# Kernel tuning notes

Measured on AMD Instinct MI355X. Metric: run time of the kernel, lower is better.

## Reference

```python
import jax, jax.numpy as jnp
import numpy as np

N_HEADS = 8
EPS = 1e-5

def _mha(q_in, kv_in, wq, bq, wk, bk, wv, bv, wo, bo, causal):
    B, N, D = q_in.shape
    Dh = D // N_HEADS
    # projections (weights stored [in, out])
    Q = (q_in @ wq + bq).reshape(B, N, N_HEADS, Dh).swapaxes(1, 2)  # [B,H,N,Dh]
    K = (kv_in @ wk + bk).reshape(B, N, N_HEADS, Dh).swapaxes(1, 2)
    V = (kv_in @ wv + bv).reshape(B, N, N_HEADS, Dh).swapaxes(1, 2)
    scores = jnp.einsum('bhqd,bhkd->bhqk', Q, K) / jnp.sqrt(jnp.asarray(Dh, q_in.dtype))
    if causal:
        m = jnp.triu(jnp.ones((N, N), dtype=bool), k=1)
        scores = jnp.where(m, jnp.asarray(-jnp.inf, scores.dtype), scores)
    w = jax.nn.softmax(scores, axis=-1)
    attn = jnp.einsum('bhqk,bhkd->bhqd', w, V).swapaxes(1, 2).reshape(B, N, D)
    return attn @ wo + bo

def _ln(x, g, b):
    mu = jnp.mean(x, axis=-1, keepdims=True)
    var = jnp.var(x, axis=-1, keepdims=True)
    return (x - mu) / jnp.sqrt(var + EPS) * g + b

def setup_inputs() -> dict:
    key = jax.random.key(0)
    D, H, S = 512, 8, 4
    ks = jax.random.split(key, 32)
    def w(k, shape):
        return jax.random.normal(k, shape, dtype=jnp.float32) * 0.02
    inp = {
        'x': jax.random.normal(ks[0], (2, 2048, D), dtype=jnp.float32),
        'encoder_output': jax.random.normal(ks[1], (2, 2048, D), dtype=jnp.float32),
        # masked self-attention params
        'm_wq': w(ks[2], (D, D)), 'm_bq': jnp.zeros((D,), jnp.float32),
        'm_wk': w(ks[3], (D, D)), 'm_bk': jnp.zeros((D,), jnp.float32),
        'm_wv': w(ks[4], (D, D)), 'm_bv': jnp.zeros((D,), jnp.float32),
        'm_wo': w(ks[5], (D, D)), 'm_bo': jnp.zeros((D,), jnp.float32),
        # cross-attention params
        'c_wq': w(ks[6], (D, D)), 'c_bq': jnp.zeros((D,), jnp.float32),
        'c_wk': w(ks[7], (D, D)), 'c_bk': jnp.zeros((D,), jnp.float32),
        'c_wv': w(ks[8], (D, D)), 'c_bv': jnp.zeros((D,), jnp.float32),
        'c_wo': w(ks[9], (D, D)), 'c_bo': jnp.zeros((D,), jnp.float32),
        # layer norms
        'ln1_g': jnp.ones((D,), jnp.float32), 'ln1_b': jnp.zeros((D,), jnp.float32),
        'ln2_g': jnp.ones((D,), jnp.float32), 'ln2_b': jnp.zeros((D,), jnp.float32),
        'ln3_g': jnp.ones((D,), jnp.float32), 'ln3_b': jnp.zeros((D,), jnp.float32),
        # feed-forward (scale=4)
        'ff_w1': w(ks[10], (D, S * D)), 'ff_b1': jnp.zeros((S * D,), jnp.float32),
        'ff_w2': w(ks[11], (S * D, D)), 'ff_b2': jnp.zeros((D,), jnp.float32),
    }
    return inp

def reference(x, encoder_output,
              m_wq, m_bq, m_wk, m_bk, m_wv, m_bv, m_wo, m_bo,
              c_wq, c_bq, c_wk, c_bk, c_wv, c_bv, c_wo, c_bo,
              ln1_g, ln1_b, ln2_g, ln2_b, ln3_g, ln3_b,
              ff_w1, ff_b1, ff_w2, ff_b2):
    x = _mha(x, x, m_wq, m_bq, m_wk, m_bk, m_wv, m_bv, m_wo, m_bo, causal=True) + x
    x = _ln(x, ln1_g, ln1_b)
    x = _mha(x, encoder_output, c_wq, c_bq, c_wk, c_bk, c_wv, c_bv, c_wo, c_bo, causal=False) + x
    x = _ln(x, ln2_g, ln2_b)
    h = jax.nn.gelu(x @ ff_w1 + ff_b1, approximate=False)  # torch nn.GELU default = exact erf
    x = h @ ff_w2 + ff_b2 + x
    x = _ln(x, ln3_g, ln3_b)
    return x
```

## Files before the change

### kernel.cpp

```cpp
#include <hip/hip_runtime.h>
#include <hip/hip_bf16.h>

typedef __attribute__((ext_vector_type(8))) short short8;
typedef __attribute__((ext_vector_type(4))) float floatx4;
typedef unsigned short u16;
typedef unsigned int u32;

#define QSCALE 0.1803368801111244f

__device__ __forceinline__ u16 f2b(float f) {
    union { float f; u32 u; } v; v.f = f;
    u32 r = v.u + 0x7fffu + ((v.u >> 16) & 1u);
    return (u16)(r >> 16);
}

__device__ __forceinline__ void gload(const u16* g, u16* l) {
    __builtin_amdgcn_global_load_lds((const __attribute__((address_space(1))) void*)g,
                                     (__attribute__((address_space(3))) void*)l, 16, 0, 0);
}

struct TPent { const float* s; u16* d; int O; int dI; };
struct TP16 { TPent e[16]; };
__global__ __launch_bounds__(256) void transpose_convert16(TP16 p) {
    __shared__ float t[32][33];
    TPent e = p.e[blockIdx.z];
    int o0 = blockIdx.x * 32, i0 = blockIdx.y * 32;
    int tx = threadIdx.x, ty = threadIdx.y;
#pragma unroll
    for (int k = 0; k < 32; k += 8) t[ty + k][tx] = e.s[(size_t)(i0 + ty + k) * e.O + o0 + tx];
    __syncthreads();
#pragma unroll
    for (int k = 0; k < 32; k += 8) e.d[(size_t)(o0 + ty + k) * e.dI + i0 + tx] = f2b(t[tx][ty + k]);
}

__global__ __launch_bounds__(256) void gather_bias(const float* b0, const float* b1, const float* b2,
                                                   const float* b3, const float* b4,
                                                   float* dqkv, float* dkv) {
    int i = blockIdx.x * 256 + threadIdx.x;
    if      (i < 512)  dqkv[i] = b0[i];
    else if (i < 1024) dqkv[i] = b1[i - 512];
    else if (i < 1536) dqkv[i] = b2[i - 1024];
    else if (i < 2048) dkv[i - 1536] = b3[i - 1536];
    else               dkv[i - 1536] = b4[i - 2048];
}

__global__ __launch_bounds__(256) void cvt_bf16_2(const float4* __restrict__ s0, ushort4* __restrict__ d0,
                                                  const float4* __restrict__ s1, ushort4* __restrict__ d1) {
    int i = blockIdx.x * 256 + threadIdx.x;
    float4 v = s0[i];
    ushort4 o; o.x = f2b(v.x); o.y = f2b(v.y); o.z = f2b(v.z); o.w = f2b(v.w);
    d0[i] = o;
    v = s1[i];
    o.x = f2b(v.x); o.y = f2b(v.y); o.z = f2b(v.z); o.w = f2b(v.w);
    d1[i] = o;
}

__global__ __launch_bounds__(256) void gemm64x128(
    const u16* __restrict__ A, int lda,
    const u16* __restrict__ B, int ldb,
    int K,
    const float* __restrict__ bias,
    const float* __restrict__ residual,
    float* __restrict__ out_f, u16* __restrict__ out_b,
    int out_stride, int scale_ncols, int gelu_flag)
{
    __shared__ u16 lA[64 * 32];
    __shared__ u16 lB[128 * 32];
    int tid = threadIdx.x, wave = tid >> 6, lane = tid & 63;
    int g4 = lane >> 4, c16 = lane & 15;
    int bm = blockIdx.x * 64, bn = blockIdx.y * 128;
    int wm = (wave >> 1) * 32, wn = (wave & 1) * 64;
    int srow = tid >> 2, skseg = (tid & 3) * 8;
    const u16* Ar = A + (size_t)(bm + srow) * lda + skseg;
    const u16* Br = B + (size_t)(bn + srow) * ldb + skseg;
    size_t b64o = (size_t)64 * ldb;

    floatx4 acc[2][4];
#pragma unroll
    for (int i = 0; i < 2; i++)
#pragma unroll
        for (int j = 0; j < 4; j++) acc[i][j] = (floatx4){0.f, 0.f, 0.f, 0.f};

    for (int kt = 0; kt < K; kt += 32) {
        __syncthreads();
        gload(Ar + kt,        lA + wave * 512);
        gload(Br + kt,        lB + wave * 512);
        gload(Br + kt + b64o, lB + 2048 + wave * 512);
        __syncthreads();
        short8 aF[2], bF[4];
#pragma unroll
        for (int i = 0; i < 2; i++) aF[i] = *(const short8*)&lA[(wm + i * 16 + c16) * 32 + g4 * 8];
#pragma unroll
        for (int j = 0; j < 4; j++) bF[j] = *(const short8*)&lB[(wn + j * 16 + c16) * 32 + g4 * 8];
#pragma unroll
        for (int i = 0; i < 2; i++)
#pragma unroll
            for (int j = 0; j < 4; j++)
                acc[i][j] = __builtin_amdgcn_mfma_f32_16x16x32_bf16(aF[i], bF[j], acc[i][j], 0, 0, 0);
    }

#pragma unroll
    for (int i = 0; i < 2; i++) {
        int row0 = bm + wm + i * 16 + g4 * 4;
#pragma unroll
        for (int j = 0; j < 4; j++) {
            int col = bn + wn + j * 16 + c16;
            float bv = bias[col];
#pragma unroll
            for (int r = 0; r < 4; r++) {
                int row = row0 + r;
                float v = acc[i][j][r] + bv;
                if (col < scale_ncols) v *= QSCALE;
                if (gelu_flag) v = 0.5f * v * (1.f + erff(v * 0.70710678118654752f));
                if (residual) v += residual[(size_t)row * out_stride + col];
                if (out_f) out_f[(size_t)row * out_stride + col] = v;
                else       out_b[(size_t)row * out_stride + col] = f2b(v);
            }
        }
    }
}

__global__ __launch_bounds__(256) void gemm64x128_dual(
    const u16* __restrict__ A0, const u16* __restrict__ B0, const float* __restrict__ bias0,
    u16* __restrict__ out0, int ostride0, int scale0,
    const u16* __restrict__ A1, const u16* __restrict__ B1, const float* __restrict__ bias1,
    u16* __restrict__ out1, int ostride1,
    int ys, int K, int lda, int ldb)
{
    __shared__ u16 lA[64 * 32];
    __shared__ u16 lB[128 * 32];
    int tid = threadIdx.x, wave = tid >> 6, lane = tid & 63;
    int g4 = lane >> 4, c16 = lane & 15;
    int by = blockIdx.y;
    const u16* A; const u16* B; const float* bias; u16* out; int ostride, scaleN, bn;
    if (by < ys) { A = A0; B = B0; bias = bias0; out = out0; ostride = ostride0; scaleN = scale0; bn = by * 128; }
    else         { A = A1; B = B1; bias = bias1; out = out1; ostride = ostride1; scaleN = 0;      bn = (by - ys) * 128; }
    int bm = blockIdx.x * 64;
    int wm = (wave >> 1) * 32, wn = (wave & 1) * 64;
    int srow = tid >> 2, skseg = (tid & 3) * 8;
    const u16* Ar = A + (size_t)(bm + srow) * lda + skseg;
    const u16* Br = B + (size_t)(bn + srow) * ldb + skseg;
    size_t b64o = (size_t)64 * ldb;

    floatx4 acc[2][4];
#pragma unroll
    for (int i = 0; i < 2; i++)
#pragma unroll
        for (int j = 0; j < 4; j++) acc[i][j] = (floatx4){0.f, 0.f, 0.f, 0.f};

    for (int kt = 0; kt < K; kt += 32) {
        __syncthreads();
        gload(Ar + kt,        lA + wave * 512);
        gload(Br + kt,        lB + wave * 512);
        gload(Br + kt + b64o, lB + 2048 + wave * 512);
        __syncthreads();
        short8 aF[2], bF[4];
#pragma unroll
        for (int i = 0; i < 2; i++) aF[i] = *(const short8*)&lA[(wm + i * 16 + c16) * 32 + g4 * 8];
#pragma unroll
        for (int j = 0; j < 4; j++) bF[j] = *(const short8*)&lB[(wn + j * 16 + c16) * 32 + g4 * 8];
#pragma unroll
        for (int i = 0; i < 2; i++)
#pragma unroll
            for (int j = 0; j < 4; j++)
                acc[i][j] = __builtin_amdgcn_mfma_f32_16x16x32_bf16(aF[i], bF[j], acc[i][j], 0, 0, 0);
    }

#pragma unroll
    for (int i = 0; i < 2; i++) {
        int row0 = bm + wm + i * 16 + g4 * 4;
#pragma unroll
        for (int j = 0; j < 4; j++) {
            int col = bn + wn + j * 16 + c16;
            float bv = bias[col];
#pragma unroll
            for (int r = 0; r < 4; r++) {
                float v = acc[i][j][r] + bv;
                if (col < scaleN) v *= QSCALE;
                out[(size_t)(row0 + r) * ostride + col] = f2b(v);
            }
        }
    }
}

__global__ __launch_bounds__(256) void gemm64x64(
    const u16* __restrict__ A, int lda,
    const u16* __restrict__ B, int ldb,
    int K,
    const float* __restrict__ bias,
    const float* __restrict__ residual,
    float* __restrict__ out_f, u16* __restrict__ out_b,
    int out_stride, int scale_ncols)
{
    __shared__ u16 lA[64 * 32];
    __shared__ u16 lB[64 * 32];
    int tid = threadIdx.x, wave = tid >> 6, lane = tid & 63;
    int g4 = lane >> 4, c16 = lane & 15;
    int bm = blockIdx.x * 64, bn = blockIdx.y * 64;
    int wm = wave * 16;
    int srow = tid >> 2, skseg = (tid & 3) * 8;
    const u16* Ar = A + (size_t)(bm + srow) * lda + skseg;
    const u16* Br = B + (size_t)(bn + srow) * ldb + skseg;

    floatx4 acc[4];
#pragma unroll
    for (int j = 0; j < 4; j++) acc[j] = (floatx4){0.f, 0.f, 0.f, 0.f};

    for (int kt = 0; kt < K; kt += 32) {
        __syncthreads();
        gload(Ar + kt, lA + wave * 512);
        gload(Br + kt, lB + wave * 512);
        __syncthreads();
        short8 aF = *(const short8*)&lA[(wm + c16) * 32 + g4 * 8];
        short8 bF[4];
#pragma unroll
        for (int j = 0; j < 4; j++) bF[j] = *(const short8*)&lB[(j * 16 + c16) * 32 + g4 * 8];
#pragma unroll
        for (int j = 0; j < 4; j++)
            acc[j] = __builtin_amdgcn_mfma_f32_16x16x32_bf16(aF, bF[j], acc[j], 0, 0, 0);
    }

    int row0 = bm + wm + g4 * 4;
#pragma unroll
    for (int j = 0; j < 4; j++) {
        int col = bn + j * 16 + c16;
        float bv = bias[col];
#pragma unroll
        for (int r = 0; r < 4; r++) {
            int row = row0 + r;
            float v = acc[j][r] + bv;
            if (col < scale_ncols) v *= QSCALE;
            if (residual) v += residual[(size_t)row * out_stride + col];
            if (out_f) out_f[(size_t)row * out_stride + col] = v;
            else       out_b[(size_t)row * out_stride + col] = f2b(v);
        }
    }
}

__global__ __launch_bounds__(256) void attn_fused(
    const u16* __restrict__ Qp, int q_stride,
    const u16* __restrict__ Kp, int kv_stride,
    const u16* __restrict__ Vp,
    float* __restrict__ Opart,
    float* __restrict__ Lpart,
    int causal)
{
    __shared__ u16 lK[64 * 72];
    __shared__ u16 lVT[64 * 72];
    __shared__ u16 lP[4 * 16 * 72];
    int tid = threadIdx.x, wave = tid >> 6, lane = tid & 63;
    int g4 = lane >> 4, c16 = lane & 15;
    int qt = blockIdx.x, bh = blockIdx.y, sp = blockIdx.z;
    size_t rowbase = (size_t)(bh >> 3) * 2048;
    int hoff = (bh & 7) * 64;
    const u16* Q = Qp + rowbase * q_stride + hoff;
    const u16* K = Kp + rowbase * kv_stride + hoff;
    const u16* V = Vp + rowbase * kv_stride + hoff;

    int qrow0 = qt * 64 + wave * 16;
    short8 qf0 = *(const short8*)&Q[(size_t)(qrow0 + c16) * q_stride + g4 * 8];
    short8 qf1 = *(const short8*)&Q[(size_t)(qrow0 + c16) * q_stride + g4 * 8 + 32];

    int kr = tid >> 2, ks = (tid & 3) * 16;
    const u16* Kbase = K + (size_t)kr * kv_stride + ks;
    int vk0 = (tid >> 3) * 2, vs = (tid & 7) * 8;
    const u16* Vbase = V + (size_t)vk0 * kv_stride + vs;

    int4 kv0, kv1, vv0, vv1;
    auto load_tile = [&](int kt) {
        const u16* kp = Kbase + (size_t)kt * 64 * kv_stride;
        kv0 = *(const int4*)(kp);
        kv1 = *(const int4*)(kp + 8);
        const u16* vp = Vbase + (size_t)kt * 64 * kv_stride;
        vv0 = *(const int4*)(vp);
        vv1 = *(const int4*)(vp + kv_stride);
    };
    auto store_tile = [&]() {
        *(int4*)&lK[kr * 72 + ks] = kv0;
        *(int4*)&lK[kr * 72 + ks + 8] = kv1;
        const u16* pa = (const u16*)&vv0;
        const u16* pb = (const u16*)&vv1;
#pragma unroll
        for (int j = 0; j < 8; j++) {
            int dh = vs + j;
            int keyS = vk0 ^ (((dh >> 3) & 3) << 4);
            u32 w = (u32)pa[j] | ((u32)pb[j] << 16);
            *(u32*)&lVT[dh * 72 + keyS] = w;
        }
    };

    floatx4 o_acc[4];
#pragma unroll
    for (int d = 0; d < 4; d++) o_acc[d] = (floatx4){0.f, 0.f, 0.f, 0.f};
    float lsum = 0.f;
    u16* lPw = lP + wave * 1152;

    int ktend = causal ? (qt + 1) : 32;
    int kt = sp;
    if (kt < ktend) load_tile(kt);

    for (; kt < ktend; kt += 2) {
        __syncthreads();
        store_tile();
        __syncthreads();
        if (kt + 2 < ktend) load_tile(kt + 2);

        floatx4 sc[4];
#pragma unroll
        for (int nt = 0; nt < 4; nt++) {
            short8 b0 = *(const short8*)&lK[(nt * 16 + c16) * 72 + g4 * 8];
            short8 b1 = *(const short8*)&lK[(nt * 16 + c16) * 72 + g4 * 8 + 32];
            floatx4 z = (floatx4){0.f, 0.f, 0.f, 0.f};
            z = __builtin_amdgcn_mfma_f32_16x16x32_bf16(b0, qf0, z, 0, 0, 0);
            z = __builtin_amdgcn_mfma_f32_16x16x32_bf16(b1, qf1, z, 0, 0, 0);
            sc[nt] = z;
        }
        if (causal && kt == qt) {
            int qr = qt * 64 + wave * 16 + c16;
#pragma unroll
            for (int nt = 0; nt < 4; nt++) {
                int key0 = kt * 64 + nt * 16 + 4 * g4;
#pragma unroll
                for (int r = 0; r < 4; r++)
                    if (key0 + r > qr) sc[nt][r] = -1e30f;
            }
        }
#pragma unroll
        for (int nt = 0; nt < 4; nt++) {
            float p0 = exp2f(sc[nt][0]);
            float p1 = exp2f(sc[nt][1]);
            float p2 = exp2f(sc[nt][2]);
            float p3 = exp2f(sc[nt][3]);
            lsum += (p0 + p1) + (p2 + p3);
            __hip_bfloat162 w0 = __float22bfloat162_rn(make_float2(p0, p1));
            __hip_bfloat162 w1 = __float22bfloat162_rn(make_float2(p2, p3));
            uint2 pk; pk.x = *(u32*)&w0; pk.y = *(u32*)&w1;
            *(uint2*)&lPw[c16 * 72 + nt * 16 + 4 * g4] = pk;
        }
        short8 pa0 = *(const short8*)&lPw[c16 * 72 + g4 * 8];
        short8 pa1 = *(const short8*)&lPw[c16 * 72 + g4 * 8 + 32];
#pragma unroll
        for (int d = 0; d < 4; d++) {
            int swz = ((2 * d + (c16 >> 3)) & 3) << 4;
            short8 vb0 = *(const short8*)&lVT[(d * 16 + c16) * 72 + ((g4 * 8) ^ swz)];
            short8 vb1 = *(const short8*)&lVT[(d * 16 + c16) * 72 + ((32 + g4 * 8) ^ swz)];
            o_acc[d] = __builtin_amdgcn_mfma_f32_16x16x32_bf16(pa0, vb0, o_acc[d], 0, 0, 0);
            o_acc[d] = __builtin_amdgcn_mfma_f32_16x16x32_bf16(pa1, vb1, o_acc[d], 0, 0, 0);
        }
    }

    lsum += __shfl_xor(lsum, 16);
    lsum += __shfl_xor(lsum, 32);
    size_t slab = (size_t)(sp * 16 + bh) * 2048;
    if (g4 == 0) Lpart[slab + qrow0 + c16] = lsum;
    float* Ob = Opart + (slab + qrow0) * 64;
#pragma unroll
    for (int d = 0; d < 4; d++)
#pragma unroll
        for (int r = 0; r < 4; r++)
            Ob[(size_t)(4 * g4 + r) * 64 + d * 16 + c16] = o_acc[d][r];
}

__global__ __launch_bounds__(256) void attn_combine(
    const float4* __restrict__ Op,
    const float* __restrict__ Lp,
    ushort4* __restrict__ out)
{
    int e = blockIdx.x * 256 + threadIdx.x;
    int dh4 = e & 15;
    int qrow = (e >> 4) & 2047;
    int bh = e >> 15;
    float l = Lp[bh * 2048 + qrow] + Lp[32768 + bh * 2048 + qrow];
    float inv = 1.f / l;
    float4 a = Op[e];
    float4 b = Op[524288 + e];
    ushort4 o;
    o.x = f2b((a.x + b.x) * inv);
    o.y = f2b((a.y + b.y) * inv);
    o.z = f2b((a.z + b.z) * inv);
    o.w = f2b((a.w + b.w) * inv);
    int row = (bh >> 3) * 2048 + qrow;
    out[(size_t)row * 128 + (bh & 7) * 16 + dh4] = o;
}

__global__ __launch_bounds__(256) void ln_kernel(const float* __restrict__ in,
                                                 const float* __restrict__ g,
                                                 const float* __restrict__ b,
                                                 float* __restrict__ out_f,
                                                 u16* __restrict__ out_b)
{
    const int D = 512;
    int row = blockIdx.x, tid = threadIdx.x;
    const float* x = in + (size_t)row * D;
    float v0 = x[tid], v1 = x[tid + 256];
    float s = v0 + v1, ss = v0 * v0 + v1 * v1;
#pragma unroll
    for (int off = 1; off < 64; off <<= 1) { s += __shfl_xor(s, off); ss += __shfl_xor(ss, off); }
    __shared__ float red[8];
    int wave = tid >> 6, lane = tid & 63;
    if (lane == 0) { red[wave] = s; red[4 + wave] = ss; }
    __syncthreads();
    float st = red[0] + red[1] + red[2] + red[3];
    float sst = red[4] + red[5] + red[6] + red[7];
    float mu = st * (1.f / 512.f);
    float var = sst * (1.f / 512.f) - mu * mu;
    float rs = rsqrtf(var + 1e-5f);
    float y0 = (v0 - mu) * rs * g[tid] + b[tid];
    float y1 = (v1 - mu) * rs * g[tid + 256] + b[tid + 256];
    if (out_f) { out_f[(size_t)row * D + tid] = y0; out_f[(size_t)row * D + tid + 256] = y1; }
    if (out_b) { out_b[(size_t)row * D + tid] = f2b(y0); out_b[(size_t)row * D + tid + 256] = f2b(y1); }
}

extern "C" void kernel_launch(void* const* d_in, const int* in_sizes, int n_in,
                              void* d_out, int out_size, void* d_ws, size_t ws_size,
                              hipStream_t stream)
{
    (void)in_sizes; (void)n_in; (void)out_size; (void)ws_size;
    const float* x     = (const float*)d_in[0];
    const float* enc   = (const float*)d_in[1];
    const float* m_wq  = (const float*)d_in[2];  const float* m_bq = (const float*)d_in[3];
    const float* m_wk  = (const float*)d_in[4];  const float* m_bk = (const float*)d_in[5];
    const float* m_wv  = (const float*)d_in[6];  const float* m_bv = (const float*)d_in[7];
    const float* m_wo  = (const float*)d_in[8];  const float* m_bo = (const float*)d_in[9];
    const float* c_wq  = (const float*)d_in[10]; const float* c_bq = (const float*)d_in[11];
    const float* c_wk  = (const float*)d_in[12]; const float* c_bk = (const float*)d_in[13];
    const float* c_wv  = (const float*)d_in[14]; const float* c_bv = (const float*)d_in[15];
    const float* c_wo  = (const float*)d_in[16]; const float* c_bo = (const float*)d_in[17];
    const float* ln1_g = (const float*)d_in[18]; const float* ln1_b = (const float*)d_in[19];
    const float* ln2_g = (const float*)d_in[20]; const float* ln2_b = (const float*)d_in[21];
    const float* ln3_g = (const float*)d_in[22]; const float* ln3_b = (const float*)d_in[23];
    const float* ff_w1 = (const float*)d_in[24]; const float* ff_b1 = (const float*)d_in[25];
    const float* ff_w2 = (const float*)d_in[26]; const float* ff_b2 = (const float*)d_in[27];

    char* base = (char*)d_ws; size_t off = 0;
    auto alloc = [&](size_t bytes) -> void* {
        void* p = base + off; off = (off + bytes + 255) & ~(size_t)255; return p;
    };
    u16*   Wqkv_m = (u16*)alloc(1536 * 512 * 2);
    u16*   Wo_m   = (u16*)alloc(512 * 512 * 2);
    u16*   Wq_c   = (u16*)alloc(512 * 512 * 2);
    u16*   Wkv_c  = (u16*)alloc(1024 * 512 * 2);
    u16*   Wo_c   = (u16*)alloc(512 * 512 * 2);
    u16*   W1t    = (u16*)alloc(2048 * 512 * 2);
    u16*   W2t    = (u16*)alloc(512 * 2048 * 2);
    float* bqkv_m = (float*)alloc(1536 * 4);
    float* bkv_c  = (float*)alloc(1024 * 4);
    u16*   xb     = (u16*)alloc((size_t)4096 * 512 * 2);
    u16*   encb   = (u16*)alloc((size_t)4096 * 512 * 2);
    u16*   qkvm   = (u16*)alloc((size_t)4096 * 1536 * 2);
    u16*   attnm  = (u16*)alloc((size_t)4096 * 512 * 2);
    float* y      = (float*)alloc((size_t)4096 * 512 * 4);
    float* x1f    = (float*)alloc((size_t)4096 * 512 * 4);
    u16*   x1b    = (u16*)alloc((size_t)4096 * 512 * 2);
    u16*   qc     = (u16*)alloc((size_t)4096 * 512 * 2);
    u16*   kvc    = (u16*)alloc((size_t)4096 * 1024 * 2);
    u16*   attnc  = (u16*)alloc((size_t)4096 * 512 * 2);
    float* x2f    = (float*)alloc((size_t)4096 * 512 * 4);
    u16*   x2b    = (u16*)alloc((size_t)4096 * 512 * 2);
    u16*   h      = (u16*)alloc((size_t)4096 * 2048 * 2);
    float* Opart  = (float*)alloc((size_t)2 * 16 * 2048 * 64 * 4);
    float* Lpart  = (float*)alloc((size_t)2 * 16 * 2048 * 4);

    TP16 tp;
    tp.e[0] = {m_wq, Wqkv_m,              512, 512};
    tp.e[1] = {m_wk, Wqkv_m + 512 * 512,  512, 512};
    tp.e[2] = {m_wv, Wqkv_m + 1024 * 512, 512, 512};
    tp.e[3] = {m_wo, Wo_m,                512, 512};
    tp.e[4] = {c_wq, Wq_c,                512, 512};
    tp.e[5] = {c_wk, Wkv_c,               512, 512};
    tp.e[6] = {c_wv, Wkv_c + 512 * 512,   512, 512};
    tp.e[7] = {c_wo, Wo_c,                512, 512};
    for (int k = 0; k < 4; k++)
        tp.e[8 + k]  = {ff_w1 + 512 * k,        W1t + k * 512 * 512, 2048, 512};
    for (int k = 0; k < 4; k++)
        tp.e[12 + k] = {ff_w2 + (size_t)512 * k * 512, W2t + 512 * k, 512, 2048};
    transpose_convert16<<<dim3(16, 16, 16), dim3(32, 8), 0, stream>>>(tp);
    gather_bias<<<10, 256, 0, stream>>>(m_bq, m_bk, m_bv, c_bk, c_bv, bqkv_m, bkv_c);
    cvt_bf16_2<<<2048, 256, 0, stream>>>((const float4*)x, (ushort4*)xb,
                                         (const float4*)enc, (ushort4*)encb);

    gemm64x128_dual<<<dim3(64, 20), 256, 0, stream>>>(
        xb, Wqkv_m, bqkv_m, qkvm, 1536, 512,
        encb, Wkv_c, bkv_c, kvc, 1024,
        12, 512, 512, 512);

    attn_fused<<<dim3(32, 16, 2), 256, 0, stream>>>(qkvm, 1536, qkvm + 512, 1536, qkvm + 1024,
                                                    Opart, Lpart, 1);
    attn_combine<<<2048, 256, 0, stream>>>((const float4*)Opart, Lpart, (ushort4*)attnm);
    gemm64x64<<<dim3(64, 8), 256, 0, stream>>>(attnm, 512, Wo_m, 512, 512,
                                               m_bo, x, y, nullptr, 512, 0);
    ln_kernel<<<4096, 256, 0, stream>>>(y, ln1_g, ln1_b, x1f, x1b);

    gemm64x64<<<dim3(64, 8), 256, 0, stream>>>(x1b, 512, Wq_c, 512, 512,
                                               c_bq, nullptr, nullptr, qc, 512, 512);
    attn_fused<<<dim3(32, 16, 2), 256, 0, stream>>>(qc, 512, kvc, 1024, kvc + 512,
                                                    Opart, Lpart, 0);
    attn_combine<<<2048, 256, 0, stream>>>((const float4*)Opart, Lpart, (ushort4*)attnc);
    gemm64x64<<<dim3(64, 8), 256, 0, stream>>>(attnc, 512, Wo_c, 512, 512,
                                               c_bo, x1f, y, nullptr, 512, 0);
    ln_kernel<<<4096, 256, 0, stream>>>(y, ln2_g, ln2_b, x2f, x2b);

    gemm64x128<<<dim3(64, 16), 256, 0, stream>>>(x2b, 512, W1t, 512, 512,
                                                 ff_b1, nullptr, nullptr, h, 2048, 0, 1);
    gemm64x64<<<dim3(64, 8), 256, 0, stream>>>(h, 2048, W2t, 2048, 2048,
                                               ff_b2, x2f, y, nullptr, 512, 0);
    ln_kernel<<<4096, 256, 0, stream>>>(y, ln3_g, ln3_b, (float*)d_out, nullptr);
}
```

Before: 352.6 us.

## Process two 64-row query tiles per attention block to reuse K/V tiles

Each attention block now handles 128 query rows as two 64-row sub-tiles that share every K/V tile staged in LDS, and the grid is halved in x. This halves global K/V loads and LDS staging per query row. The causal path skips the first sub-tile's work on the extra diagonal tile. In exchange, accumulator registers double, which may lower occupancy, and there are fewer blocks to balance the triangular causal workload.

```diff
diff --git a/kernel.cpp b/kernel.cpp
--- a/kernel.cpp
+++ b/kernel.cpp
@@ -257,9 +257,12 @@
     const u16* K = Kp + rowbase * kv_stride + hoff;
     const u16* V = Vp + rowbase * kv_stride + hoff;
 
-    int qrow0 = qt * 64 + wave * 16;
-    short8 qf0 = *(const short8*)&Q[(size_t)(qrow0 + c16) * q_stride + g4 * 8];
-    short8 qf1 = *(const short8*)&Q[(size_t)(qrow0 + c16) * q_stride + g4 * 8 + 32];
+    int qrowA0 = qt * 128 + wave * 16;
+    int qrowB0 = qrowA0 + 64;
+    short8 qfA0 = *(const short8*)&Q[(size_t)(qrowA0 + c16) * q_stride + g4 * 8];
+    short8 qfA1 = *(const short8*)&Q[(size_t)(qrowA0 + c16) * q_stride + g4 * 8 + 32];
+    short8 qfB0 = *(const short8*)&Q[(size_t)(qrowB0 + c16) * q_stride + g4 * 8];
+    short8 qfB1 = *(const short8*)&Q[(size_t)(qrowB0 + c16) * q_stride + g4 * 8 + 32];
 
     int kr = tid >> 2, ks = (tid & 3) * 16;
     const u16* Kbase = K + (size_t)kr * kv_stride + ks;
@@ -289,13 +292,16 @@
         }
     };
 
-    floatx4 o_acc[4];
-#pragma unroll
-    for (int d = 0; d < 4; d++) o_acc[d] = (floatx4){0.f, 0.f, 0.f, 0.f};
-    float lsum = 0.f;
+    floatx4 o_accA[4], o_accB[4];
+#pragma unroll
+    for (int d = 0; d < 4; d++) {
+        o_accA[d] = (floatx4){0.f, 0.f, 0.f, 0.f};
+        o_accB[d] = (floatx4){0.f, 0.f, 0.f, 0.f};
+    }
+    float lsumA = 0.f, lsumB = 0.f;
     u16* lPw = lP + wave * 1152;
 
-    int ktend = causal ? (qt + 1) : 32;
+    int ktend = causal ? (2 * qt + 2) : 32;
     int kt = sp;
     if (kt < ktend) load_tile(kt);
 
@@ -305,60 +311,109 @@
         __syncthreads();
         if (kt + 2 < ktend) load_tile(kt + 2);
 
-        floatx4 sc[4];
+        bool skipA = causal && (kt > 2 * qt);
+        bool maskA = causal && (kt == 2 * qt);
+        bool maskB = causal && (kt == 2 * qt + 1);
+
+        floatx4 scA[4], scB[4];
 #pragma unroll
         for (int nt = 0; nt < 4; nt++) {
             short8 b0 = *(const short8*)&lK[(nt * 16 + c16) * 72 + g4 * 8];
             short8 b1 = *(const short8*)&lK[(nt * 16 + c16) * 72 + g4 * 8 + 32];
+            if (!skipA) {
+                floatx4 z = (floatx4){0.f, 0.f, 0.f, 0.f};
+                z = __builtin_amdgcn_mfma_f32_16x16x32_bf16(b0, qfA0, z, 0, 0, 0);
+                z = __builtin_amdgcn_mfma_f32_16x16x32_bf16(b1, qfA1, z, 0, 0, 0);
+                scA[nt] = z;
+            }
             floatx4 z = (floatx4){0.f, 0.f, 0.f, 0.f};
-            z = __builtin_amdgcn_mfma_f32_16x16x32_bf16(b0, qf0, z, 0, 0, 0);
-            z = __builtin_amdgcn_mfma_f32_16x16x32_bf16(b1, qf1, z, 0, 0, 0);
-            sc[nt] = z;
-        }
-        if (causal && kt == qt) {
-            int qr = qt * 64 + wave * 16 + c16;
+            z = __builtin_amdgcn_mfma_f32_16x16x32_bf16(b0, qfB0, z, 0, 0, 0);
+            z = __builtin_amdgcn_mfma_f32_16x16x32_bf16(b1, qfB1, z, 0, 0, 0);
+            scB[nt] = z;
+        }
+        if (maskA) {
+            int qr = qrowA0 + c16;
 #pragma unroll
             for (int nt = 0; nt < 4; nt++) {
                 int key0 = kt * 64 + nt * 16 + 4 * g4;
 #pragma unroll
                 for (int r = 0; r < 4; r++)
-                    if (key0 + r > qr) sc[nt][r] = -1e30f;
-            }
+                    if (key0 + r > qr) scA[nt][r] = -1e30f;
+            }
+        }
+        if (maskB) {
+            int qr = qrowB0 + c16;
+#pragma unroll
+            for (int nt = 0; nt < 4; nt++) {
+                int key0 = kt * 64 + nt * 16 + 4 * g4;
+#pragma unroll
+                for (int r = 0; r < 4; r++)
+                    if (key0 + r > qr) scB[nt][r] = -1e30f;
+            }
+        }
+
+        short8 paA0, paA1, paB0, paB1;
+        if (!skipA) {
+#pragma unroll
+            for (int nt = 0; nt < 4; nt++) {
+                float p0 = exp2f(scA[nt][0]);
+                float p1 = exp2f(scA[nt][1]);
+                float p2 = exp2f(scA[nt][2]);
+                float p3 = exp2f(scA[nt][3]);
+                lsumA += (p0 + p1) + (p2 + p3);
+                __hip_bfloat162 w0 = __float22bfloat162_rn(make_float2(p0, p1));
+                __hip_bfloat162 w1 = __float22bfloat162_rn(make_float2(p2, p3));
+                uint2 pk; pk.x = *(u32*)&w0; pk.y = *(u32*)&w1;
+                *(uint2*)&lPw[c16 * 72 + nt * 16 + 4 * g4] = pk;
+            }
+            paA0 = *(const short8*)&lPw[c16 * 72 + g4 * 8];
+            paA1 = *(const short8*)&lPw[c16 * 72 + g4 * 8 + 32];
         }
 #pragma unroll
         for (int nt = 0; nt < 4; nt++) {
-            float p0 = exp2f(sc[nt][0]);
-            float p1 = exp2f(sc[nt][1]);
-            float p2 = exp2f(sc[nt][2]);
-            float p3 = exp2f(sc[nt][3]);
-            lsum += (p0 + p1) + (p2 + p3);
+            float p0 = exp2f(scB[nt][0]);
+            float p1 = exp2f(scB[nt][1]);
+            float p2 = exp2f(scB[nt][2]);
+            float p3 = exp2f(scB[nt][3]);
+            lsumB += (p0 + p1) + (p2 + p3);
             __hip_bfloat162 w0 = __float22bfloat162_rn(make_float2(p0, p1));
             __hip_bfloat162 w1 = __float22bfloat162_rn(make_float2(p2, p3));
             uint2 pk; pk.x = *(u32*)&w0; pk.y = *(u32*)&w1;
             *(uint2*)&lPw[c16 * 72 + nt * 16 + 4 * g4] = pk;
         }
-        short8 pa0 = *(const short8*)&lPw[c16 * 72 + g4 * 8];
-        short8 pa1 = *(const short8*)&lPw[c16 * 72 + g4 * 8 + 32];
+        paB0 = *(const short8*)&lPw[c16 * 72 + g4 * 8];
+        paB1 = *(const short8*)&lPw[c16 * 72 + g4 * 8 + 32];
+
 #pragma unroll
         for (int d = 0; d < 4; d++) {
             int swz = ((2 * d + (c16 >> 3)) & 3) << 4;
             short8 vb0 = *(const short8*)&lVT[(d * 16 + c16) * 72 + ((g4 * 8) ^ swz)];
             short8 vb1 = *(const short8*)&lVT[(d * 16 + c16) * 72 + ((32 + g4 * 8) ^ swz)];
-            o_acc[d] = __builtin_amdgcn_mfma_f32_16x16x32_bf16(pa0, vb0, o_acc[d], 0, 0, 0);
-            o_acc[d] = __builtin_amdgcn_mfma_f32_16x16x32_bf16(pa1, vb1, o_acc[d], 0, 0, 0);
-        }
-    }
-
-    lsum += __shfl_xor(lsum, 16);
-    lsum += __shfl_xor(lsum, 32);
+            if (!skipA) {
+                o_accA[d] = __builtin_amdgcn_mfma_f32_16x16x32_bf16(paA0, vb0, o_accA[d], 0, 0, 0);
+                o_accA[d] = __builtin_amdgcn_mfma_f32_16x16x32_bf16(paA1, vb1, o_accA[d], 0, 0, 0);
+            }
+            o_accB[d] = __builtin_amdgcn_mfma_f32_16x16x32_bf16(paB0, vb0, o_accB[d], 0, 0, 0);
+            o_accB[d] = __builtin_amdgcn_mfma_f32_16x16x32_bf16(paB1, vb1, o_accB[d], 0, 0, 0);
+        }
+    }
+
+    lsumA += __shfl_xor(lsumA, 16); lsumA += __shfl_xor(lsumA, 32);
+    lsumB += __shfl_xor(lsumB, 16); lsumB += __shfl_xor(lsumB, 32);
     size_t slab = (size_t)(sp * 16 + bh) * 2048;
-    if (g4 == 0) Lpart[slab + qrow0 + c16] = lsum;
-    float* Ob = Opart + (slab + qrow0) * 64;
+    if (g4 == 0) {
+        Lpart[slab + qrowA0 + c16] = lsumA;
+        Lpart[slab + qrowB0 + c16] = lsumB;
+    }
+    float* ObA = Opart + (slab + qrowA0) * 64;
+    float* ObB = Opart + (slab + qrowB0) * 64;
 #pragma unroll
     for (int d = 0; d < 4; d++)
 #pragma unroll
-        for (int r = 0; r < 4; r++)
-            Ob[(size_t)(4 * g4 + r) * 64 + d * 16 + c16] = o_acc[d][r];
+        for (int r = 0; r < 4; r++) {
+            ObA[(size_t)(4 * g4 + r) * 64 + d * 16 + c16] = o_accA[d][r];
+            ObB[(size_t)(4 * g4 + r) * 64 + d * 16 + c16] = o_accB[d][r];
+        }
 }
 
 __global__ __launch_bounds__(256) void attn_combine(
@@ -484,7 +539,7 @@
         encb, Wkv_c, bkv_c, kvc, 1024,
         12, 512, 512, 512);
 
-    attn_fused<<<dim3(32, 16, 2), 256, 0, stream>>>(qkvm, 1536, qkvm + 512, 1536, qkvm + 1024,
+    attn_fused<<<dim3(16, 16, 2), 256, 0, stream>>>(qkvm, 1536, qkvm + 512, 1536, qkvm + 1024,
                                                     Opart, Lpart, 1);
     attn_combine<<<2048, 256, 0, stream>>>((const float4*)Opart, Lpart, (ushort4*)attnm);
     gemm64x64<<<dim3(64, 8), 256, 0, stream>>>(attnm, 512, Wo_m, 512, 512,
@@ -493,7 +548,7 @@
 
     gemm64x64<<<dim3(64, 8), 256, 0, stream>>>(x1b, 512, Wq_c, 512, 512,
                                                c_bq, nullptr, nullptr, qc, 512, 512);
-    attn_fused<<<dim3(32, 16, 2), 256, 0, stream>>>(qc, 512, kvc, 1024, kvc + 512,
+    attn_fused<<<dim3(16, 16, 2), 256, 0, stream>>>(qc, 512, kvc, 1024, kvc + 512,
                                                     Opart, Lpart, 0);
     attn_combine<<<2048, 256, 0, stream>>>((const float4*)Opart, Lpart, (ushort4*)attnc);
     gemm64x64<<<dim3(64, 8), 256, 0, stream>>>(attnc, 512, Wo_c, 512, 512,
```

New measurement: 412.4 us. 17.0% more time.

## Split-K output GEMMs with LN-side reduction and 4-way attention key split

Applied to the files above, without the earlier changes.

Adds a split-K 64x64 GEMM that writes two partial sums, which the layernorm kernel now adds before normalizing. This doubles the block count for the N=512 projection and FFN-down GEMMs, which otherwise launch only 512 blocks. Attention also splits the key range four ways instead of two, and the combine kernel sums four partials. The cost is extra partial-buffer traffic in global memory and a simpler GEMM mainloop with no double buffering.

```diff
diff --git a/kernel.cpp b/kernel.cpp
--- a/kernel.cpp
+++ b/kernel.cpp
@@ -237,6 +237,58 @@
     }
 }
 
+__global__ __launch_bounds__(256) void gemm64x64s(
+    const u16* __restrict__ A, int lda,
+    const u16* __restrict__ B, int ldb,
+    int Ksub,
+    const float* __restrict__ bias,
+    const float* __restrict__ residual,
+    float* __restrict__ out0, int out_stride)
+{
+    __shared__ u16 lA[64 * 32];
+    __shared__ u16 lB[64 * 32];
+    int tid = threadIdx.x, wave = tid >> 6, lane = tid & 63;
+    int g4 = lane >> 4, c16 = lane & 15;
+    int bm = blockIdx.x * 64, bn = blockIdx.y * 64, sp = blockIdx.z;
+    int wm = wave * 16;
+    int srow = tid >> 2, skseg = (tid & 3) * 8 + sp * Ksub;
+    const u16* Ar = A + (size_t)(bm + srow) * lda + skseg;
+    const u16* Br = B + (size_t)(bn + srow) * ldb + skseg;
+
+    floatx4 acc[4];
+#pragma unroll
+    for (int j = 0; j < 4; j++) acc[j] = (floatx4){0.f, 0.f, 0.f, 0.f};
+
+    for (int kt = 0; kt < Ksub; kt += 32) {
+        __syncthreads();
+        gload(Ar + kt, lA + wave * 512);
+        gload(Br + kt, lB + wave * 512);
+        __syncthreads();
+        short8 aF = *(const short8*)&lA[(wm + c16) * 32 + g4 * 8];
+        short8 bF[4];
+#pragma unroll
+        for (int j = 0; j < 4; j++) bF[j] = *(const short8*)&lB[(j * 16 + c16) * 32 + g4 * 8];
+#pragma unroll
+        for (int j = 0; j < 4; j++)
+            acc[j] = __builtin_amdgcn_mfma_f32_16x16x32_bf16(aF, bF[j], acc[j], 0, 0, 0);
+    }
+
+    float* out = out0 + (size_t)sp * 4096 * 512;
+    int row0 = bm + wm + g4 * 4;
+#pragma unroll
+    for (int j = 0; j < 4; j++) {
+        int col = bn + j * 16 + c16;
+        float bv = (sp == 0) ? bias[col] : 0.f;
+#pragma unroll
+        for (int r = 0; r < 4; r++) {
+            int row = row0 + r;
+            float v = acc[j][r] + bv;
+            if (sp == 0 && residual) v += residual[(size_t)row * out_stride + col];
+            out[(size_t)row * out_stride + col] = v;
+        }
+    }
+}
+
 __global__ __launch_bounds__(256) void attn_fused(
     const u16* __restrict__ Qp, int q_stride,
     const u16* __restrict__ Kp, int kv_stride,
@@ -299,11 +351,11 @@
     int kt = sp;
     if (kt < ktend) load_tile(kt);
 
-    for (; kt < ktend; kt += 2) {
+    for (; kt < ktend; kt += 4) {
         __syncthreads();
         store_tile();
         __syncthreads();
-        if (kt + 2 < ktend) load_tile(kt + 2);
+        if (kt + 4 < ktend) load_tile(kt + 4);
 
         floatx4 sc[4];
 #pragma unroll
@@ -370,20 +422,24 @@
     int dh4 = e & 15;
     int qrow = (e >> 4) & 2047;
     int bh = e >> 15;
-    float l = Lp[bh * 2048 + qrow] + Lp[32768 + bh * 2048 + qrow];
+    int li = bh * 2048 + qrow;
+    float l = Lp[li] + Lp[32768 + li] + Lp[65536 + li] + Lp[98304 + li];
     float inv = 1.f / l;
     float4 a = Op[e];
     float4 b = Op[524288 + e];
+    float4 c = Op[1048576 + e];
+    float4 d = Op[1572864 + e];
     ushort4 o;
-    o.x = f2b((a.x + b.x) * inv);
-    o.y = f2b((a.y + b.y) * inv);
-    o.z = f2b((a.z + b.z) * inv);
-    o.w = f2b((a.w + b.w) * inv);
+    o.x = f2b((a.x + b.x + c.x + d.x) * inv);
+    o.y = f2b((a.y + b.y + c.y + d.y) * inv);
+    o.z = f2b((a.z + b.z + c.z + d.z) * inv);
+    o.w = f2b((a.w + b.w + c.w + d.w) * inv);
     int row = (bh >> 3) * 2048 + qrow;
     out[(size_t)row * 128 + (bh & 7) * 16 + dh4] = o;
 }
 
-__global__ __launch_bounds__(256) void ln_kernel(const float* __restrict__ in,
+__global__ __launch_bounds__(256) void ln_kernel(const float* __restrict__ in0,
+                                                 const float* __restrict__ in1,
                                                  const float* __restrict__ g,
                                                  const float* __restrict__ b,
                                                  float* __restrict__ out_f,
@@ -391,8 +447,9 @@
 {
     const int D = 512;
     int row = blockIdx.x, tid = threadIdx.x;
-    const float* x = in + (size_t)row * D;
-    float v0 = x[tid], v1 = x[tid + 256];
+    size_t base = (size_t)row * D;
+    float v0 = in0[base + tid], v1 = in0[base + tid + 256];
+    if (in1) { v0 += in1[base + tid]; v1 += in1[base + tid + 256]; }
     float s = v0 + v1, ss = v0 * v0 + v1 * v1;
 #pragma unroll
     for (int off = 1; off < 64; off <<= 1) { s += __shfl_xor(s, off); ss += __shfl_xor(ss, off); }
@@ -407,8 +464,8 @@
     float rs = rsqrtf(var + 1e-5f);
     float y0 = (v0 - mu) * rs * g[tid] + b[tid];
     float y1 = (v1 - mu) * rs * g[tid + 256] + b[tid + 256];
-    if (out_f) { out_f[(size_t)row * D + tid] = y0; out_f[(size_t)row * D + tid + 256] = y1; }
-    if (out_b) { out_b[(size_t)row * D + tid] = f2b(y0); out_b[(size_t)row * D + tid + 256] = f2b(y1); }
+    if (out_f) { out_f[base + tid] = y0; out_f[base + tid + 256] = y1; }
+    if (out_b) { out_b[base + tid] = f2b(y0); out_b[base + tid + 256] = f2b(y1); }
 }
 
 extern "C" void kernel_launch(void* const* d_in, const int* in_sizes, int n_in,
@@ -449,7 +506,7 @@
     u16*   encb   = (u16*)alloc((size_t)4096 * 512 * 2);
     u16*   qkvm   = (u16*)alloc((size_t)4096 * 1536 * 2);
     u16*   attnm  = (u16*)alloc((size_t)4096 * 512 * 2);
-    float* y      = (float*)alloc((size_t)4096 * 512 * 4);
+    float* y01    = (float*)alloc((size_t)2 * 4096 * 512 * 4);
     float* x1f    = (float*)alloc((size_t)4096 * 512 * 4);
     u16*   x1b    = (u16*)alloc((size_t)4096 * 512 * 2);
     u16*   qc     = (u16*)alloc((size_t)4096 * 512 * 2);
@@ -458,8 +515,8 @@
     float* x2f    = (float*)alloc((size_t)4096 * 512 * 4);
     u16*   x2b    = (u16*)alloc((size_t)4096 * 512 * 2);
     u16*   h      = (u16*)alloc((size_t)4096 * 2048 * 2);
-    float* Opart  = (float*)alloc((size_t)2 * 16 * 2048 * 64 * 4);
-    float* Lpart  = (float*)alloc((size_t)2 * 16 * 2048 * 4);
+    float* Opart  = (float*)alloc((size_t)4 * 16 * 2048 * 64 * 4);
+    float* Lpart  = (float*)alloc((size_t)4 * 16 * 2048 * 4);
 
     TP16 tp;
     tp.e[0] = {m_wq, Wqkv_m,              512, 512};
@@ -484,25 +541,26 @@
         encb, Wkv_c, bkv_c, kvc, 1024,
         12, 512, 512, 512);
 
-    attn_fused<<<dim3(32, 16, 2), 256, 0, stream>>>(qkvm, 1536, qkvm + 512, 1536, qkvm + 1024,
+    attn_fused<<<dim3(32, 16, 4), 256, 0, stream>>>(qkvm, 1536, qkvm + 512, 1536, qkvm + 1024,
                                                     Opart, Lpart, 1);
     attn_combine<<<2048, 256, 0, stream>>>((const float4*)Opart, Lpart, (ushort4*)attnm);
-    gemm64x64<<<dim3(64, 8), 256, 0, stream>>>(attnm, 512, Wo_m, 512, 512,
-                                               m_bo, x, y, nullptr, 512, 0);
-    ln_kernel<<<4096, 256, 0, stream>>>(y, ln1_g, ln1_b, x1f, x1b);
+    gemm64x64s<<<dim3(64, 8, 2), 256, 0, stream>>>(attnm, 512, Wo_m, 512, 256,
+                                                   m_bo, x, y01, 512);
+    ln_kernel<<<4096, 256, 0, stream>>>(y01, y01 + (size_t)4096 * 512, ln1_g, ln1_b, x1f, x1b);
 
     gemm64x64<<<dim3(64, 8), 256, 0, stream>>>(x1b, 512, Wq_c, 512, 512,
                                                c_bq, nullptr, nullptr, qc, 512, 512);
-    attn_fused<<<dim3(32, 16, 2), 256, 0, stream>>>(qc, 512, kvc, 1024, kvc + 512,
+    attn_fused<<<dim3(32, 16, 4), 256, 0, stream>>>(qc, 512, kvc, 1024, kvc + 512,
                                                     Opart, Lpart, 0);
     attn_combine<<<2048, 256, 0, stream>>>((const float4*)Opart, Lpart, (ushort4*)attnc);
-    gemm64x64<<<dim3(64, 8), 256, 0, stream>>>(attnc, 512, Wo_c, 512, 512,
-                                               c_bo, x1f, y, nullptr, 512, 0);
-    ln_kernel<<<4096, 256, 0, stream>>>(y, ln2_g, ln2_b, x2f, x2b);
+    gemm64x64s<<<dim3(64, 8, 2), 256, 0, stream>>>(attnc, 512, Wo_c, 512, 256,
+                                                   c_bo, x1f, y01, 512);
+    ln_kernel<<<4096, 256, 0, stream>>>(y01, y01 + (size_t)4096 * 512, ln2_g, ln2_b, x2f, x2b);
 
     gemm64x128<<<dim3(64, 16), 256, 0, stream>>>(x2b, 512, W1t, 512, 512,
                                                  ff_b1, nullptr, nullptr, h, 2048, 0, 1);
-    gemm64x64<<<dim3(64, 8), 256, 0, stream>>>(h, 2048, W2t, 2048, 2048,
-                                               ff_b2, x2f, y, nullptr, 512, 0);
-    ln_kernel<<<4096, 256, 0, stream>>>(y, ln3_g, ln3_b, (float*)d_out, nullptr);
-}
+    gemm64x64s<<<dim3(64, 8, 2), 256, 0, stream>>>(h, 2048, W2t, 2048, 1024,
+                                                   ff_b2, x2f, y01, 512);
+    ln_kernel<<<4096, 256, 0, stream>>>(y01, y01 + (size_t)4096 * 512, ln3_g, ln3_b,
+                                        (float*)d_out, nullptr);
+}
```

New measurement: 342.6 us. 1.03x faster.
